# Performance work log

Measured on AMD Instinct MI355X. Metric: run time of the kernel, lower is better.

The kernel has to match this reference:

```python
import jax, jax.numpy as jnp
import numpy as np
from math import sqrt

HEADS = 16
DIM_HEAD = 64
BETA = 1.0 / sqrt(DIM_HEAD)


def setup_inputs() -> dict:
    key = jax.random.key(0)
    k1, k2, k3 = jax.random.split(key, 3)
    b, n, dim = 2, 2048, 1024
    inner = HEADS * DIM_HEAD  # 1024
    x = jax.random.normal(k1, (b, n, dim), dtype=jnp.float32)
    W_qk = jax.random.normal(k2, (dim, 2 * inner), dtype=jnp.float32) * 0.02
    W_out = jax.random.normal(k3, (inner, dim), dtype=jnp.float32) * 0.02
    return {"x": x, "W_qk": W_qk, "W_out": W_out}


def reference(x, W_qk, W_out):
    # x: [b, n, dim]; to_qk: Linear(dim, 2*inner, bias=False)
    b, n, _ = x.shape
    qk = x @ W_qk                                   # [b, n, 2*inner]
    q, k = jnp.split(qk, 2, axis=-1)                # each [b, n, inner]
    # b n (h d) -> b h n d
    q = q.reshape(b, n, HEADS, DIM_HEAD).transpose(0, 2, 1, 3)
    k = k.reshape(b, n, HEADS, DIM_HEAD).transpose(0, 2, 1, 3)
    # beta-scaled scores
    scores = jnp.einsum('bhid,bhjd->bhij', q * BETA, k)  # [b, h, n, n]
    mask_value = -jnp.finfo(scores.dtype).max
    causal_mask = jnp.triu(jnp.ones((n, n), dtype=bool), k=1)
    scores = jnp.where(causal_mask, mask_value, scores)
    attn = jax.nn.softmax(scores, axis=-1)
    # K is reused as V
    out = jnp.einsum('bhij,bhjd->bhid', attn, k)    # [b, h, n, d]
    out = out.transpose(0, 2, 1, 3).reshape(b, n, HEADS * DIM_HEAD)
    # to_out Linear (dropout is identity in eval)
    return out @ W_out
```

## Files before the change

kernel.cpp:

```cpp
#include <hip/hip_runtime.h>
#include <hip/hip_bf16.h>
#include <math.h>

typedef short bf16x8 __attribute__((ext_vector_type(8)));
typedef float f32x4 __attribute__((ext_vector_type(4)));

__device__ __forceinline__ float bf2f(unsigned short u) {
    return __uint_as_float(((unsigned int)u) << 16);
}
__device__ __forceinline__ unsigned short f2bf(float f) {
    unsigned int u = __float_as_uint(f);
    u = (u + 0x7FFFu + ((u >> 16) & 1u)) >> 16;
    return (unsigned short)u;
}
__device__ __forceinline__ unsigned int pk2bf(float a, float b) {
    __hip_bfloat162 u = __float22bfloat162_rn(make_float2(a, b));
    return *(unsigned int*)&u;
}

#define ASYNC16(gp, lp)                                                        \
    __builtin_amdgcn_global_load_lds(                                          \
        (const __attribute__((address_space(1))) unsigned int*)(gp),           \
        (__attribute__((address_space(3))) unsigned int*)(lp), 16, 0, 0)

__global__ __launch_bounds__(256) void cast_x_kernel(const float* __restrict__ in,
                                                     unsigned short* __restrict__ out, int n) {
    int i = (blockIdx.x * 256 + threadIdx.x) * 8;
    if (i >= n) return;
    float4 a = *(const float4*)(in + i);
    float4 b = *(const float4*)(in + i + 4);
    bf16x8 v;
    v[0] = (short)f2bf(a.x); v[1] = (short)f2bf(a.y); v[2] = (short)f2bf(a.z); v[3] = (short)f2bf(a.w);
    v[4] = (short)f2bf(b.x); v[5] = (short)f2bf(b.y); v[6] = (short)f2bf(b.z); v[7] = (short)f2bf(b.w);
    *(bf16x8*)(out + i) = v;
}

__global__ __launch_bounds__(256) void transpose_cast_kernel(const float* __restrict__ in,
                                                             unsigned short* __restrict__ out,
                                                             int K, int N) {
    __shared__ float tile[32][33];
    int k0 = blockIdx.x * 32, n0 = blockIdx.y * 32;
    int tx = threadIdx.x & 31, ty = threadIdx.x >> 5;
    #pragma unroll
    for (int i = ty; i < 32; i += 8)
        tile[i][tx] = in[(size_t)(k0 + i) * N + (n0 + tx)];
    __syncthreads();
    #pragma unroll
    for (int i = ty; i < 32; i += 8)
        out[(size_t)(n0 + i) * K + (k0 + tx)] = f2bf(tile[tx][i]);
}

__global__ __launch_bounds__(256) void ktrans_kernel(const unsigned short* __restrict__ qkb,
                                                     unsigned short* __restrict__ kT) {
    __shared__ unsigned short tl[64][68];
    const int b = blockIdx.z;
    const int tok0 = blockIdx.x * 64;
    const int f0 = blockIdx.y * 64;
    const int r = threadIdx.x >> 4;
    const int c = (threadIdx.x & 15) * 4;
    #pragma unroll
    for (int i = 0; i < 4; ++i) {
        const int rr = r + 16 * i;
        ushort4 v = *(const ushort4*)(qkb + ((size_t)(b * 2048 + tok0 + rr)) * 2048 + 1024 + f0 + c);
        *(ushort4*)&tl[rr][c] = v;
    }
    __syncthreads();
    #pragma unroll
    for (int i = 0; i < 4; ++i) {
        const int fr = r + 16 * i;
        ushort4 v;
        v.x = tl[c + 0][fr]; v.y = tl[c + 1][fr]; v.z = tl[c + 2][fr]; v.w = tl[c + 3][fr];
        *(ushort4*)(kT + ((size_t)(b * 1024 + f0 + fr)) * 2048 + tok0 + c) = v;
    }
}

template <bool STORE_BF16>
__global__ __launch_bounds__(256) void gemm128_kernel(const unsigned short* __restrict__ A,
                                                      const unsigned short* __restrict__ Bt,
                                                      void* __restrict__ C,
                                                      int K, int lda, int ldb, int ldc) {
    __shared__ unsigned short As[128 * 32];
    __shared__ unsigned short Bs[128 * 32];
    const int tid = threadIdx.x;
    const int wave = tid >> 6;
    const int lane = tid & 63;
    const int quad = lane >> 4;
    const int col  = lane & 15;
    const int wm = (wave >> 1) * 64;
    const int wn = (wave & 1) * 64;
    const int m0 = blockIdx.x * 128, n0 = blockIdx.y * 128;

    f32x4 acc[4][4];
    #pragma unroll
    for (int i = 0; i < 4; ++i)
        #pragma unroll
        for (int j = 0; j < 4; ++j) { acc[i][j][0] = 0.f; acc[i][j][1] = 0.f; acc[i][j][2] = 0.f; acc[i][j][3] = 0.f; }

    const int srow = tid >> 2;
    const int skc  = (tid & 3) * 8;

    for (int k0 = 0; k0 < K; k0 += 32) {
        __syncthreads();
        const unsigned short* ga = A  + (size_t)(m0 + srow) * lda + k0 + skc;
        const unsigned short* gb = Bt + (size_t)(n0 + srow) * ldb + k0 + skc;
        ASYNC16(ga,            &As[wave * 512]);
        ASYNC16(ga + 64 * lda, &As[2048 + wave * 512]);
        ASYNC16(gb,            &Bs[wave * 512]);
        ASYNC16(gb + 64 * ldb, &Bs[2048 + wave * 512]);
        __syncthreads();

        bf16x8 af[4], bf[4];
        #pragma unroll
        for (int mf = 0; mf < 4; ++mf)
            af[mf] = *(const bf16x8*)&As[(wm + mf * 16 + col) * 32 + quad * 8];
        #pragma unroll
        for (int nf = 0; nf < 4; ++nf)
            bf[nf] = *(const bf16x8*)&Bs[(wn + nf * 16 + col) * 32 + quad * 8];
        #pragma unroll
        for (int mf = 0; mf < 4; ++mf)
            #pragma unroll
            for (int nf = 0; nf < 4; ++nf)
                acc[mf][nf] = __builtin_amdgcn_mfma_f32_16x16x32_bf16(af[mf], bf[nf], acc[mf][nf], 0, 0, 0);
    }

    #pragma unroll
    for (int mf = 0; mf < 4; ++mf) {
        const int row0 = m0 + wm + mf * 16 + quad * 4;
        #pragma unroll
        for (int nf = 0; nf < 4; ++nf) {
            const int cc = n0 + wn + nf * 16 + col;
            #pragma unroll
            for (int r = 0; r < 4; ++r) {
                if (STORE_BF16)
                    ((unsigned short*)C)[(size_t)(row0 + r) * ldc + cc] = f2bf(acc[mf][nf][r]);
                else
                    ((float*)C)[(size_t)(row0 + r) * ldc + cc] = acc[mf][nf][r];
            }
        }
    }
}

#define LDK 72

__global__ __launch_bounds__(256) void attn_v5_kernel(const unsigned short* __restrict__ qkb,
                                                      const unsigned short* __restrict__ kT,
                                                      unsigned short* __restrict__ aout) {
    __shared__ unsigned short Kbuf[2][2][64 * 64];
    __shared__ unsigned short Ps[4][16 * LDK];

    const int bh = blockIdx.x;
    const int b = bh >> 4, h = bh & 15;
    const int qtile = 31 - (int)blockIdx.y;
    const int tid = threadIdx.x;
    const int wave = tid >> 6, lane = tid & 63, quad = lane >> 4, col = lane & 15;

    bf16x8 qa0, qa1;
    {
        const unsigned short* qp =
            qkb + ((size_t)(b * 2048 + qtile * 64 + wave * 16 + col)) * 2048 + h * 64;
        bf16x8 r0 = *(const bf16x8*)(qp + quad * 8);
        bf16x8 r1 = *(const bf16x8*)(qp + 32 + quad * 8);
        const float sc = 0.125f * 1.44269504088896f;
        #pragma unroll
        for (int i = 0; i < 8; ++i) {
            qa0[i] = (short)f2bf(bf2f((unsigned short)r0[i]) * sc);
            qa1[i] = (short)f2bf(bf2f((unsigned short)r1[i]) * sc);
        }
    }

    f32x4 accO[4];
    #pragma unroll
    for (int t = 0; t < 4; ++t) { accO[t][0] = 0.f; accO[t][1] = 0.f; accO[t][2] = 0.f; accO[t][3] = 0.f; }
    float lsum = 0.f;

    const int r8 = lane >> 3;
    const int c8 = (lane & 7) ^ r8;
    const unsigned short* knp =
        qkb + ((size_t)(b * 2048 + wave * 16 + r8)) * 2048 + 1024 + h * 64 + c8 * 8;
    const unsigned short* ktp = kT + ((size_t)(bh * 64 + wave * 16 + r8)) * 2048 + c8 * 8;

    auto issue = [&](int jt, int p) {
        const unsigned short* kn = knp + (size_t)jt * 64 * 2048;
        const unsigned short* kt = ktp + jt * 64;
        unsigned short* knl = &Kbuf[p][0][(wave * 16) * 64];
        unsigned short* ktl = &Kbuf[p][1][(wave * 16) * 64];
        ASYNC16(kn,            knl);
        ASYNC16(kn + 8 * 2048, knl + 8 * 64);
        ASYNC16(kt,            ktl);
        ASYNC16(kt + 8 * 2048, ktl + 8 * 64);
    };

    issue(0, 0);

    for (int jt = 0; jt <= qtile; ++jt) {
        const int cur = jt & 1;
        __builtin_amdgcn_s_barrier();
        if (jt < qtile) issue(jt + 1, cur ^ 1);
        if (jt < qtile) __builtin_amdgcn_s_waitcnt(0xF74);
        else            __builtin_amdgcn_s_waitcnt(0xF70);
        __builtin_amdgcn_s_barrier();
        __asm__ volatile("" ::: "memory");

        const unsigned short* Knc = &Kbuf[cur][0][0];
        const unsigned short* Ktc = &Kbuf[cur][1][0];

        const bool diag = (jt == qtile);
        const int tmax = diag ? wave : 3;

        float ls = 0.f;
        unsigned int pw[4][2];
        #pragma unroll
        for (int t = 0; t < 4; ++t) {
            if (t <= tmax) {
                const int row = (t * 16 + col) * 64;
                const int sw = col & 7;
                bf16x8 ka0 = *(const bf16x8*)&Knc[row + (quad ^ sw) * 8];
                bf16x8 ka1 = *(const bf16x8*)&Knc[row + ((4 + quad) ^ sw) * 8];
                f32x4 c = {-16.f, -16.f, -16.f, -16.f};
                c = __builtin_amdgcn_mfma_f32_16x16x32_bf16(ka0, qa0, c, 0, 0, 0);
                c = __builtin_amdgcn_mfma_f32_16x16x32_bf16(ka1, qa1, c, 0, 0, 0);
                if (diag && t == wave) {
                    #pragma unroll
                    for (int r = 0; r < 4; ++r)
                        if (quad * 4 + r > col) c[r] = -1e30f;
                }
                const float p0 = exp2f(c[0]);
                const float p1 = exp2f(c[1]);
                const float p2 = exp2f(c[2]);
                const float p3 = exp2f(c[3]);
                ls += (p0 + p1) + (p2 + p3);
                pw[t][0] = pk2bf(p0, p1);
                pw[t][1] = pk2bf(p2, p3);
            } else {
                pw[t][0] = 0u; pw[t][1] = 0u;
            }
        }
        lsum += ls;

        unsigned short* psb = &Ps[wave][col * LDK];
        #pragma unroll
        for (int t = 0; t < 4; ++t)
            *(uint2*)(psb + t * 16 + quad * 4) = make_uint2(pw[t][0], pw[t][1]);

        bf16x8 pa0 = *(const bf16x8*)(psb + quad * 8);
        bf16x8 pa1 = *(const bf16x8*)(psb + 32 + quad * 8);
        const bool hi = !(diag && wave < 2);

        #pragma unroll
        for (int t = 0; t < 4; ++t) {
            const int row = (t * 16 + col) * 64;
            const int sw = col & 7;
            bf16x8 vb0 = *(const bf16x8*)&Ktc[row + (quad ^ sw) * 8];
            accO[t] = __builtin_amdgcn_mfma_f32_16x16x32_bf16(pa0, vb0, accO[t], 0, 0, 0);
            if (hi) {
                bf16x8 vb1 = *(const bf16x8*)&Ktc[row + ((4 + quad) ^ sw) * 8];
                accO[t] = __builtin_amdgcn_mfma_f32_16x16x32_bf16(pa1, vb1, accO[t], 0, 0, 0);
            }
        }
    }

    lsum += __shfl_xor(lsum, 16);
    lsum += __shfl_xor(lsum, 32);
    #pragma unroll
    for (int r = 0; r < 4; ++r) {
        const float lr = __shfl(lsum, (lane & 48) | (quad * 4 + r));
        const float inv = 1.f / lr;
        const size_t row = (size_t)b * 2048 + qtile * 64 + wave * 16 + quad * 4 + r;
        unsigned short* op = aout + row * 1024 + h * 64;
        op[col]      = f2bf(accO[0][r] * inv);
        op[16 + col] = f2bf(accO[1][r] * inv);
        op[32 + col] = f2bf(accO[2][r] * inv);
        op[48 + col] = f2bf(accO[3][r] * inv);
    }
}

extern "C" void kernel_launch(void* const* d_in, const int* in_sizes, int n_in,
                              void* d_out, int out_size, void* d_ws, size_t ws_size,
                              hipStream_t stream) {
    (void)in_sizes; (void)n_in; (void)out_size; (void)ws_size;
    const float* x    = (const float*)d_in[0];
    const float* Wqk  = (const float*)d_in[1];
    const float* Wout = (const float*)d_in[2];
    float* out = (float*)d_out;

    unsigned short* xb     = (unsigned short*)d_ws;
    unsigned short* Wqk_t  = xb     + (size_t)4096 * 1024;
    unsigned short* Wout_t = Wqk_t  + (size_t)2048 * 1024;
    unsigned short* qkb    = Wout_t + (size_t)1024 * 1024;
    unsigned short* aoutb  = qkb    + (size_t)4096 * 2048;
    unsigned short* kT     = xb;

    cast_x_kernel<<<dim3(4096 * 1024 / (256 * 8)), dim3(256), 0, stream>>>(x, xb, 4096 * 1024);
    transpose_cast_kernel<<<dim3(32, 64), dim3(256), 0, stream>>>(Wqk, Wqk_t, 1024, 2048);
    transpose_cast_kernel<<<dim3(32, 32), dim3(256), 0, stream>>>(Wout, Wout_t, 1024, 1024);

    gemm128_kernel<true><<<dim3(32, 16), dim3(256), 0, stream>>>(
        xb, Wqk_t, (void*)qkb, 1024, 1024, 1024, 2048);

    ktrans_kernel<<<dim3(32, 16, 2), dim3(256), 0, stream>>>(qkb, kT);

    attn_v5_kernel<<<dim3(32, 32), dim3(256), 0, stream>>>(qkb, kT, aoutb);

    gemm128_kernel<false><<<dim3(32, 8), dim3(256), 0, stream>>>(
        aoutb, Wout_t, (void*)out, 1024, 1024, 1024, 1024);
}
```

Baseline: 194.8 us.

## Use 128-row query tiles in attention and 128x64 GEMM tiles

```diff
diff --git a/kernel.cpp b/kernel.cpp
--- a/kernel.cpp
+++ b/kernel.cpp
@@ -75,26 +75,26 @@
 }
 
 template <bool STORE_BF16>
-__global__ __launch_bounds__(256) void gemm128_kernel(const unsigned short* __restrict__ A,
-                                                      const unsigned short* __restrict__ Bt,
-                                                      void* __restrict__ C,
-                                                      int K, int lda, int ldb, int ldc) {
+__global__ __launch_bounds__(256) void gemm12864_kernel(const unsigned short* __restrict__ A,
+                                                        const unsigned short* __restrict__ Bt,
+                                                        void* __restrict__ C,
+                                                        int K, int lda, int ldb, int ldc) {
     __shared__ unsigned short As[128 * 32];
-    __shared__ unsigned short Bs[128 * 32];
+    __shared__ unsigned short Bs[64 * 32];
     const int tid = threadIdx.x;
     const int wave = tid >> 6;
     const int lane = tid & 63;
     const int quad = lane >> 4;
     const int col  = lane & 15;
     const int wm = (wave >> 1) * 64;
-    const int wn = (wave & 1) * 64;
-    const int m0 = blockIdx.x * 128, n0 = blockIdx.y * 128;
-
-    f32x4 acc[4][4];
+    const int wn = (wave & 1) * 32;
+    const int m0 = blockIdx.x * 128, n0 = blockIdx.y * 64;
+
+    f32x4 acc[4][2];
     #pragma unroll
     for (int i = 0; i < 4; ++i)
         #pragma unroll
-        for (int j = 0; j < 4; ++j) { acc[i][j][0] = 0.f; acc[i][j][1] = 0.f; acc[i][j][2] = 0.f; acc[i][j][3] = 0.f; }
+        for (int j = 0; j < 2; ++j) { acc[i][j][0] = 0.f; acc[i][j][1] = 0.f; acc[i][j][2] = 0.f; acc[i][j][3] = 0.f; }
 
     const int srow = tid >> 2;
     const int skc  = (tid & 3) * 8;
@@ -106,20 +106,19 @@
         ASYNC16(ga,            &As[wave * 512]);
         ASYNC16(ga + 64 * lda, &As[2048 + wave * 512]);
         ASYNC16(gb,            &Bs[wave * 512]);
-        ASYNC16(gb + 64 * ldb, &Bs[2048 + wave * 512]);
         __syncthreads();
 
-        bf16x8 af[4], bf[4];
+        bf16x8 af[4], bf[2];
         #pragma unroll
         for (int mf = 0; mf < 4; ++mf)
             af[mf] = *(const bf16x8*)&As[(wm + mf * 16 + col) * 32 + quad * 8];
         #pragma unroll
-        for (int nf = 0; nf < 4; ++nf)
+        for (int nf = 0; nf < 2; ++nf)
             bf[nf] = *(const bf16x8*)&Bs[(wn + nf * 16 + col) * 32 + quad * 8];
         #pragma unroll
         for (int mf = 0; mf < 4; ++mf)
             #pragma unroll
-            for (int nf = 0; nf < 4; ++nf)
+            for (int nf = 0; nf < 2; ++nf)
                 acc[mf][nf] = __builtin_amdgcn_mfma_f32_16x16x32_bf16(af[mf], bf[nf], acc[mf][nf], 0, 0, 0);
     }
 
@@ -127,7 +126,7 @@
     for (int mf = 0; mf < 4; ++mf) {
         const int row0 = m0 + wm + mf * 16 + quad * 4;
         #pragma unroll
-        for (int nf = 0; nf < 4; ++nf) {
+        for (int nf = 0; nf < 2; ++nf) {
             const int cc = n0 + wn + nf * 16 + col;
             #pragma unroll
             for (int r = 0; r < 4; ++r) {
@@ -140,38 +139,42 @@
     }
 }
 
-#define LDK 72
-
-__global__ __launch_bounds__(256) void attn_v5_kernel(const unsigned short* __restrict__ qkb,
+#define PLD 68
+
+__global__ __launch_bounds__(256) void attn_v6_kernel(const unsigned short* __restrict__ qkb,
                                                       const unsigned short* __restrict__ kT,
                                                       unsigned short* __restrict__ aout) {
     __shared__ unsigned short Kbuf[2][2][64 * 64];
-    __shared__ unsigned short Ps[4][16 * LDK];
+    __shared__ unsigned short Ps[4][32 * PLD];
 
     const int bh = blockIdx.x;
     const int b = bh >> 4, h = bh & 15;
-    const int qtile = 31 - (int)blockIdx.y;
+    const int qt = 15 - (int)blockIdx.y;
     const int tid = threadIdx.x;
     const int wave = tid >> 6, lane = tid & 63, quad = lane >> 4, col = lane & 15;
-
-    bf16x8 qa0, qa1;
-    {
+    const int Q0 = qt * 128;
+
+    bf16x8 qa[2][2];
+    #pragma unroll
+    for (int g = 0; g < 2; ++g) {
         const unsigned short* qp =
-            qkb + ((size_t)(b * 2048 + qtile * 64 + wave * 16 + col)) * 2048 + h * 64;
+            qkb + ((size_t)(b * 2048 + Q0 + wave * 32 + g * 16 + col)) * 2048 + h * 64;
         bf16x8 r0 = *(const bf16x8*)(qp + quad * 8);
         bf16x8 r1 = *(const bf16x8*)(qp + 32 + quad * 8);
         const float sc = 0.125f * 1.44269504088896f;
         #pragma unroll
         for (int i = 0; i < 8; ++i) {
-            qa0[i] = (short)f2bf(bf2f((unsigned short)r0[i]) * sc);
-            qa1[i] = (short)f2bf(bf2f((unsigned short)r1[i]) * sc);
-        }
-    }
-
-    f32x4 accO[4];
-    #pragma unroll
-    for (int t = 0; t < 4; ++t) { accO[t][0] = 0.f; accO[t][1] = 0.f; accO[t][2] = 0.f; accO[t][3] = 0.f; }
-    float lsum = 0.f;
+            qa[g][0][i] = (short)f2bf(bf2f((unsigned short)r0[i]) * sc);
+            qa[g][1][i] = (short)f2bf(bf2f((unsigned short)r1[i]) * sc);
+        }
+    }
+
+    f32x4 accO[2][4];
+    #pragma unroll
+    for (int g = 0; g < 2; ++g)
+        #pragma unroll
+        for (int t = 0; t < 4; ++t) { accO[g][t][0] = 0.f; accO[g][t][1] = 0.f; accO[g][t][2] = 0.f; accO[g][t][3] = 0.f; }
+    float lsum[2] = {0.f, 0.f};
 
     const int r8 = lane >> 3;
     const int c8 = (lane & 7) ^ r8;
@@ -190,87 +193,113 @@
         ASYNC16(kt + 8 * 2048, ktl + 8 * 64);
     };
 
+    const int jtA = 2 * qt + 1;
     issue(0, 0);
 
-    for (int jt = 0; jt <= qtile; ++jt) {
+    for (int jt = 0; jt <= jtA; ++jt) {
         const int cur = jt & 1;
         __builtin_amdgcn_s_barrier();
-        if (jt < qtile) issue(jt + 1, cur ^ 1);
-        if (jt < qtile) __builtin_amdgcn_s_waitcnt(0xF74);
-        else            __builtin_amdgcn_s_waitcnt(0xF70);
+        if (jt < jtA) issue(jt + 1, cur ^ 1);
+        if (jt < jtA) __builtin_amdgcn_s_waitcnt(0xF74);
+        else          __builtin_amdgcn_s_waitcnt(0xF70);
         __builtin_amdgcn_s_barrier();
         __asm__ volatile("" ::: "memory");
 
         const unsigned short* Knc = &Kbuf[cur][0][0];
         const unsigned short* Ktc = &Kbuf[cur][1][0];
 
-        const bool diag = (jt == qtile);
-        const int tmax = diag ? wave : 3;
-
-        float ls = 0.f;
-        unsigned int pw[4][2];
+        int delta[2], tmax[2];
+        #pragma unroll
+        for (int g = 0; g < 2; ++g) {
+            delta[g] = ((2 * qt - jt) * 64 + wave * 32 + g * 16) >> 4;
+            tmax[g] = delta[g] < 3 ? delta[g] : 3;
+        }
+        if (tmax[1] < 0) continue;
+
+        const int sw = col & 7;
+        unsigned int pw[2][4][2];
         #pragma unroll
         for (int t = 0; t < 4; ++t) {
-            if (t <= tmax) {
+            if (t <= tmax[1]) {
                 const int row = (t * 16 + col) * 64;
-                const int sw = col & 7;
                 bf16x8 ka0 = *(const bf16x8*)&Knc[row + (quad ^ sw) * 8];
                 bf16x8 ka1 = *(const bf16x8*)&Knc[row + ((4 + quad) ^ sw) * 8];
-                f32x4 c = {-16.f, -16.f, -16.f, -16.f};
-                c = __builtin_amdgcn_mfma_f32_16x16x32_bf16(ka0, qa0, c, 0, 0, 0);
-                c = __builtin_amdgcn_mfma_f32_16x16x32_bf16(ka1, qa1, c, 0, 0, 0);
-                if (diag && t == wave) {
-                    #pragma unroll
-                    for (int r = 0; r < 4; ++r)
-                        if (quad * 4 + r > col) c[r] = -1e30f;
+                #pragma unroll
+                for (int g = 0; g < 2; ++g) {
+                    if (t <= tmax[g]) {
+                        f32x4 c = {-16.f, -16.f, -16.f, -16.f};
+                        c = __builtin_amdgcn_mfma_f32_16x16x32_bf16(ka0, qa[g][0], c, 0, 0, 0);
+                        c = __builtin_amdgcn_mfma_f32_16x16x32_bf16(ka1, qa[g][1], c, 0, 0, 0);
+                        if (t == delta[g]) {
+                            #pragma unroll
+                            for (int r = 0; r < 4; ++r)
+                                if (quad * 4 + r > col) c[r] = -1e30f;
+                        }
+                        const float p0 = exp2f(c[0]);
+                        const float p1 = exp2f(c[1]);
+                        const float p2 = exp2f(c[2]);
+                        const float p3 = exp2f(c[3]);
+                        lsum[g] += (p0 + p1) + (p2 + p3);
+                        pw[g][t][0] = pk2bf(p0, p1);
+                        pw[g][t][1] = pk2bf(p2, p3);
+                    } else {
+                        pw[g][t][0] = 0u; pw[g][t][1] = 0u;
+                    }
                 }
-                const float p0 = exp2f(c[0]);
-                const float p1 = exp2f(c[1]);
-                const float p2 = exp2f(c[2]);
-                const float p3 = exp2f(c[3]);
-                ls += (p0 + p1) + (p2 + p3);
-                pw[t][0] = pk2bf(p0, p1);
-                pw[t][1] = pk2bf(p2, p3);
             } else {
-                pw[t][0] = 0u; pw[t][1] = 0u;
+                pw[0][t][0] = 0u; pw[0][t][1] = 0u;
+                pw[1][t][0] = 0u; pw[1][t][1] = 0u;
             }
         }
-        lsum += ls;
-
-        unsigned short* psb = &Ps[wave][col * LDK];
-        #pragma unroll
-        for (int t = 0; t < 4; ++t)
-            *(uint2*)(psb + t * 16 + quad * 4) = make_uint2(pw[t][0], pw[t][1]);
-
-        bf16x8 pa0 = *(const bf16x8*)(psb + quad * 8);
-        bf16x8 pa1 = *(const bf16x8*)(psb + 32 + quad * 8);
-        const bool hi = !(diag && wave < 2);
+
+        bf16x8 pa[2][2];
+        #pragma unroll
+        for (int g = 0; g < 2; ++g) {
+            if (tmax[g] >= 0) {
+                unsigned short* psb = &Ps[wave][(g * 16 + col) * PLD];
+                #pragma unroll
+                for (int t = 0; t < 4; ++t)
+                    *(uint2*)(psb + t * 16 + quad * 4) = make_uint2(pw[g][t][0], pw[g][t][1]);
+                pa[g][0] = *(const bf16x8*)(psb + quad * 8);
+                pa[g][1] = *(const bf16x8*)(psb + 32 + quad * 8);
+            }
+        }
+
+        const bool alive0 = (tmax[0] >= 0);
+        const bool hi0 = (tmax[0] >= 2), hi1 = (tmax[1] >= 2);
 
         #pragma unroll
         for (int t = 0; t < 4; ++t) {
             const int row = (t * 16 + col) * 64;
-            const int sw = col & 7;
             bf16x8 vb0 = *(const bf16x8*)&Ktc[row + (quad ^ sw) * 8];
-            accO[t] = __builtin_amdgcn_mfma_f32_16x16x32_bf16(pa0, vb0, accO[t], 0, 0, 0);
-            if (hi) {
+            if (alive0)
+                accO[0][t] = __builtin_amdgcn_mfma_f32_16x16x32_bf16(pa[0][0], vb0, accO[0][t], 0, 0, 0);
+            accO[1][t] = __builtin_amdgcn_mfma_f32_16x16x32_bf16(pa[1][0], vb0, accO[1][t], 0, 0, 0);
+            if (hi1) {
                 bf16x8 vb1 = *(const bf16x8*)&Ktc[row + ((4 + quad) ^ sw) * 8];
-                accO[t] = __builtin_amdgcn_mfma_f32_16x16x32_bf16(pa1, vb1, accO[t], 0, 0, 0);
+                if (hi0)
+                    accO[0][t] = __builtin_amdgcn_mfma_f32_16x16x32_bf16(pa[0][1], vb1, accO[0][t], 0, 0, 0);
+                accO[1][t] = __builtin_amdgcn_mfma_f32_16x16x32_bf16(pa[1][1], vb1, accO[1][t], 0, 0, 0);
             }
         }
     }
 
-    lsum += __shfl_xor(lsum, 16);
-    lsum += __shfl_xor(lsum, 32);
-    #pragma unroll
-    for (int r = 0; r < 4; ++r) {
-        const float lr = __shfl(lsum, (lane & 48) | (quad * 4 + r));
-        const float inv = 1.f / lr;
-        const size_t row = (size_t)b * 2048 + qtile * 64 + wave * 16 + quad * 4 + r;
-        unsigned short* op = aout + row * 1024 + h * 64;
-        op[col]      = f2bf(accO[0][r] * inv);
-        op[16 + col] = f2bf(accO[1][r] * inv);
-        op[32 + col] = f2bf(accO[2][r] * inv);
-        op[48 + col] = f2bf(accO[3][r] * inv);
+    #pragma unroll
+    for (int g = 0; g < 2; ++g) {
+        float ls = lsum[g];
+        ls += __shfl_xor(ls, 16);
+        ls += __shfl_xor(ls, 32);
+        #pragma unroll
+        for (int r = 0; r < 4; ++r) {
+            const float lr = __shfl(ls, (lane & 48) | (quad * 4 + r));
+            const float inv = 1.f / lr;
+            const size_t row = (size_t)b * 2048 + Q0 + wave * 32 + g * 16 + quad * 4 + r;
+            unsigned short* op = aout + row * 1024 + h * 64;
+            op[col]      = f2bf(accO[g][0][r] * inv);
+            op[16 + col] = f2bf(accO[g][1][r] * inv);
+            op[32 + col] = f2bf(accO[g][2][r] * inv);
+            op[48 + col] = f2bf(accO[g][3][r] * inv);
+        }
     }
 }
 
@@ -294,13 +323,13 @@
     transpose_cast_kernel<<<dim3(32, 64), dim3(256), 0, stream>>>(Wqk, Wqk_t, 1024, 2048);
     transpose_cast_kernel<<<dim3(32, 32), dim3(256), 0, stream>>>(Wout, Wout_t, 1024, 1024);
 
-    gemm128_kernel<true><<<dim3(32, 16), dim3(256), 0, stream>>>(
+    gemm12864_kernel<true><<<dim3(32, 32), dim3(256), 0, stream>>>(
         xb, Wqk_t, (void*)qkb, 1024, 1024, 1024, 2048);
 
     ktrans_kernel<<<dim3(32, 16, 2), dim3(256), 0, stream>>>(qkb, kT);
 
-    attn_v5_kernel<<<dim3(32, 32), dim3(256), 0, stream>>>(qkb, kT, aoutb);
-
-    gemm128_kernel<false><<<dim3(32, 8), dim3(256), 0, stream>>>(
+    attn_v6_kernel<<<dim3(32, 16), dim3(256), 0, stream>>>(qkb, kT, aoutb);
+
+    gemm12864_kernel<false><<<dim3(32, 16), dim3(256), 0, stream>>>(
         aoutb, Wout_t, (void*)out, 1024, 1024, 1024, 1024);
 }
```

Result: slower. 218.6 us (+12.2%).

## Fuse x cast and K transpose into QK GEMM, merge weight transposes, use 128x64 tiles

Applied to the files above, without the earlier changes.

```diff
diff --git a/kernel.cpp b/kernel.cpp
--- a/kernel.cpp
+++ b/kernel.cpp
@@ -23,21 +23,16 @@
         (const __attribute__((address_space(1))) unsigned int*)(gp),           \
         (__attribute__((address_space(3))) unsigned int*)(lp), 16, 0, 0)
 
-__global__ __launch_bounds__(256) void cast_x_kernel(const float* __restrict__ in,
-                                                     unsigned short* __restrict__ out, int n) {
-    int i = (blockIdx.x * 256 + threadIdx.x) * 8;
-    if (i >= n) return;
-    float4 a = *(const float4*)(in + i);
-    float4 b = *(const float4*)(in + i + 4);
-    bf16x8 v;
-    v[0] = (short)f2bf(a.x); v[1] = (short)f2bf(a.y); v[2] = (short)f2bf(a.z); v[3] = (short)f2bf(a.w);
-    v[4] = (short)f2bf(b.x); v[5] = (short)f2bf(b.y); v[6] = (short)f2bf(b.z); v[7] = (short)f2bf(b.w);
-    *(bf16x8*)(out + i) = v;
-}
-
-__global__ __launch_bounds__(256) void transpose_cast_kernel(const float* __restrict__ in,
-                                                             unsigned short* __restrict__ out,
-                                                             int K, int N) {
+__global__ __launch_bounds__(256) void wtrans_kernel(const float* __restrict__ Wqk,
+                                                     const float* __restrict__ Wout,
+                                                     unsigned short* __restrict__ Wqk_t,
+                                                     unsigned short* __restrict__ Wout_t) {
+    const int z = blockIdx.z;
+    const int N = z ? 1024 : 2048;
+    if (z && blockIdx.y >= 32) return;
+    const float* in = z ? Wout : Wqk;
+    unsigned short* out = z ? Wout_t : Wqk_t;
+    const int K = 1024;
     __shared__ float tile[32][33];
     int k0 = blockIdx.x * 32, n0 = blockIdx.y * 32;
     int tx = threadIdx.x & 31, ty = threadIdx.x >> 5;
@@ -50,76 +45,69 @@
         out[(size_t)(n0 + i) * K + (k0 + tx)] = f2bf(tile[tx][i]);
 }
 
-__global__ __launch_bounds__(256) void ktrans_kernel(const unsigned short* __restrict__ qkb,
-                                                     unsigned short* __restrict__ kT) {
-    __shared__ unsigned short tl[64][68];
-    const int b = blockIdx.z;
-    const int tok0 = blockIdx.x * 64;
-    const int f0 = blockIdx.y * 64;
-    const int r = threadIdx.x >> 4;
-    const int c = (threadIdx.x & 15) * 4;
-    #pragma unroll
-    for (int i = 0; i < 4; ++i) {
-        const int rr = r + 16 * i;
-        ushort4 v = *(const ushort4*)(qkb + ((size_t)(b * 2048 + tok0 + rr)) * 2048 + 1024 + f0 + c);
-        *(ushort4*)&tl[rr][c] = v;
-    }
-    __syncthreads();
-    #pragma unroll
-    for (int i = 0; i < 4; ++i) {
-        const int fr = r + 16 * i;
-        ushort4 v;
-        v.x = tl[c + 0][fr]; v.y = tl[c + 1][fr]; v.z = tl[c + 2][fr]; v.w = tl[c + 3][fr];
-        *(ushort4*)(kT + ((size_t)(b * 1024 + f0 + fr)) * 2048 + tok0 + c) = v;
-    }
-}
-
-template <bool STORE_BF16>
-__global__ __launch_bounds__(256) void gemm128_kernel(const unsigned short* __restrict__ A,
-                                                      const unsigned short* __restrict__ Bt,
-                                                      void* __restrict__ C,
-                                                      int K, int lda, int ldb, int ldc) {
-    __shared__ unsigned short As[128 * 32];
-    __shared__ unsigned short Bs[128 * 32];
+template <bool STORE_BF16, bool A_FP32, bool WRITE_KT>
+__global__ __launch_bounds__(256) void gemm12864_kernel(const void* __restrict__ Av,
+                                                        const unsigned short* __restrict__ Bt,
+                                                        void* __restrict__ C,
+                                                        unsigned short* __restrict__ kT,
+                                                        int K, int lda, int ldb, int ldc) {
+    constexpr int ASTR = A_FP32 ? 40 : 32;
+    __shared__ unsigned short As[128 * ASTR];
+    __shared__ unsigned short Bs[64 * 32];
     const int tid = threadIdx.x;
     const int wave = tid >> 6;
     const int lane = tid & 63;
     const int quad = lane >> 4;
     const int col  = lane & 15;
     const int wm = (wave >> 1) * 64;
-    const int wn = (wave & 1) * 64;
-    const int m0 = blockIdx.x * 128, n0 = blockIdx.y * 128;
-
-    f32x4 acc[4][4];
+    const int wn = (wave & 1) * 32;
+    const int m0 = blockIdx.x * 128, n0 = blockIdx.y * 64;
+
+    f32x4 acc[4][2];
     #pragma unroll
     for (int i = 0; i < 4; ++i)
         #pragma unroll
-        for (int j = 0; j < 4; ++j) { acc[i][j][0] = 0.f; acc[i][j][1] = 0.f; acc[i][j][2] = 0.f; acc[i][j][3] = 0.f; }
+        for (int j = 0; j < 2; ++j) { acc[i][j][0] = 0.f; acc[i][j][1] = 0.f; acc[i][j][2] = 0.f; acc[i][j][3] = 0.f; }
 
     const int srow = tid >> 2;
     const int skc  = (tid & 3) * 8;
+    const int frow = tid >> 1;
+    const int fcol = (tid & 1) * 16;
 
     for (int k0 = 0; k0 < K; k0 += 32) {
         __syncthreads();
-        const unsigned short* ga = A  + (size_t)(m0 + srow) * lda + k0 + skc;
+        if (A_FP32) {
+            const float* gx = (const float*)Av + (size_t)(m0 + frow) * lda + k0 + fcol;
+            float4 f0 = *(const float4*)(gx);
+            float4 f1 = *(const float4*)(gx + 4);
+            float4 f2 = *(const float4*)(gx + 8);
+            float4 f3 = *(const float4*)(gx + 12);
+            uint4 w0 = make_uint4(pk2bf(f0.x, f0.y), pk2bf(f0.z, f0.w),
+                                  pk2bf(f1.x, f1.y), pk2bf(f1.z, f1.w));
+            uint4 w1 = make_uint4(pk2bf(f2.x, f2.y), pk2bf(f2.z, f2.w),
+                                  pk2bf(f3.x, f3.y), pk2bf(f3.z, f3.w));
+            *(uint4*)&As[frow * ASTR + fcol]     = w0;
+            *(uint4*)&As[frow * ASTR + fcol + 8] = w1;
+        } else {
+            const unsigned short* ga = (const unsigned short*)Av + (size_t)(m0 + srow) * lda + k0 + skc;
+            ASYNC16(ga,            &As[wave * 512]);
+            ASYNC16(ga + 64 * lda, &As[2048 + wave * 512]);
+        }
         const unsigned short* gb = Bt + (size_t)(n0 + srow) * ldb + k0 + skc;
-        ASYNC16(ga,            &As[wave * 512]);
-        ASYNC16(ga + 64 * lda, &As[2048 + wave * 512]);
-        ASYNC16(gb,            &Bs[wave * 512]);
-        ASYNC16(gb + 64 * ldb, &Bs[2048 + wave * 512]);
+        ASYNC16(gb, &Bs[wave * 512]);
         __syncthreads();
 
-        bf16x8 af[4], bf[4];
+        bf16x8 af[4], bf[2];
         #pragma unroll
         for (int mf = 0; mf < 4; ++mf)
-            af[mf] = *(const bf16x8*)&As[(wm + mf * 16 + col) * 32 + quad * 8];
-        #pragma unroll
-        for (int nf = 0; nf < 4; ++nf)
+            af[mf] = *(const bf16x8*)&As[(wm + mf * 16 + col) * ASTR + quad * 8];
+        #pragma unroll
+        for (int nf = 0; nf < 2; ++nf)
             bf[nf] = *(const bf16x8*)&Bs[(wn + nf * 16 + col) * 32 + quad * 8];
         #pragma unroll
         for (int mf = 0; mf < 4; ++mf)
             #pragma unroll
-            for (int nf = 0; nf < 4; ++nf)
+            for (int nf = 0; nf < 2; ++nf)
                 acc[mf][nf] = __builtin_amdgcn_mfma_f32_16x16x32_bf16(af[mf], bf[nf], acc[mf][nf], 0, 0, 0);
     }
 
@@ -127,7 +115,7 @@
     for (int mf = 0; mf < 4; ++mf) {
         const int row0 = m0 + wm + mf * 16 + quad * 4;
         #pragma unroll
-        for (int nf = 0; nf < 4; ++nf) {
+        for (int nf = 0; nf < 2; ++nf) {
             const int cc = n0 + wn + nf * 16 + col;
             #pragma unroll
             for (int r = 0; r < 4; ++r) {
@@ -135,6 +123,13 @@
                     ((unsigned short*)C)[(size_t)(row0 + r) * ldc + cc] = f2bf(acc[mf][nf][r]);
                 else
                     ((float*)C)[(size_t)(row0 + r) * ldc + cc] = acc[mf][nf][r];
+            }
+            if (WRITE_KT && cc >= 1024) {
+                const int bb = row0 >> 11, tok = row0 & 2047;
+                ushort4 v;
+                v.x = f2bf(acc[mf][nf][0]); v.y = f2bf(acc[mf][nf][1]);
+                v.z = f2bf(acc[mf][nf][2]); v.w = f2bf(acc[mf][nf][3]);
+                *(ushort4*)(kT + ((size_t)(bb * 1024 + cc - 1024)) * 2048 + tok) = v;
             }
         }
     }
@@ -283,24 +278,19 @@
     const float* Wout = (const float*)d_in[2];
     float* out = (float*)d_out;
 
-    unsigned short* xb     = (unsigned short*)d_ws;
-    unsigned short* Wqk_t  = xb     + (size_t)4096 * 1024;
+    unsigned short* kT     = (unsigned short*)d_ws;
+    unsigned short* Wqk_t  = kT     + (size_t)2048 * 2048;
     unsigned short* Wout_t = Wqk_t  + (size_t)2048 * 1024;
     unsigned short* qkb    = Wout_t + (size_t)1024 * 1024;
     unsigned short* aoutb  = qkb    + (size_t)4096 * 2048;
-    unsigned short* kT     = xb;
-
-    cast_x_kernel<<<dim3(4096 * 1024 / (256 * 8)), dim3(256), 0, stream>>>(x, xb, 4096 * 1024);
-    transpose_cast_kernel<<<dim3(32, 64), dim3(256), 0, stream>>>(Wqk, Wqk_t, 1024, 2048);
-    transpose_cast_kernel<<<dim3(32, 32), dim3(256), 0, stream>>>(Wout, Wout_t, 1024, 1024);
-
-    gemm128_kernel<true><<<dim3(32, 16), dim3(256), 0, stream>>>(
-        xb, Wqk_t, (void*)qkb, 1024, 1024, 1024, 2048);
-
-    ktrans_kernel<<<dim3(32, 16, 2), dim3(256), 0, stream>>>(qkb, kT);
+
+    wtrans_kernel<<<dim3(32, 64, 2), dim3(256), 0, stream>>>(Wqk, Wout, Wqk_t, Wout_t);
+
+    gemm12864_kernel<true, true, true><<<dim3(32, 32), dim3(256), 0, stream>>>(
+        (const void*)x, Wqk_t, (void*)qkb, kT, 1024, 1024, 1024, 2048);
 
     attn_v5_kernel<<<dim3(32, 32), dim3(256), 0, stream>>>(qkb, kT, aoutb);
 
-    gemm128_kernel<false><<<dim3(32, 8), dim3(256), 0, stream>>>(
-        aoutb, Wout_t, (void*)out, 1024, 1024, 1024, 1024);
-}
+    gemm12864_kernel<false, false, false><<<dim3(32, 16), dim3(256), 0, stream>>>(
+        (const void*)aoutb, Wout_t, (void*)out, nullptr, 1024, 1024, 1024, 1024);
+}
```

New measurement: 198.3 us. Within noise of the previous version (+1.8%).
